# Kernel tuning notes

Hardware: AMD Instinct MI355X
Metric: run time of the kernel (lower is better)

The kernel has to match this reference:

```python
import jax, jax.numpy as jnp
import numpy as np

DIM = 1024
HEADS = 16
HEAD_DIM = DIM // HEADS
HIDDEN = 4 * DIM
EPS = 1e-5


def layernorm(x, g, b):
    mu = jnp.mean(x, axis=-1, keepdims=True)
    var = jnp.var(x, axis=-1, keepdims=True)
    return (x - mu) * jax.lax.rsqrt(var + EPS) * g + b


def setup_inputs() -> dict:
    key = jax.random.key(0)
    ks = jax.random.split(key, 6)
    B, N = 4, 1024
    s = lambda fan_in: 1.0 / np.sqrt(fan_in)
    return {
        "x": jax.random.normal(ks[0], (B, N, DIM), jnp.float32),
        "ln1_g": jnp.ones((DIM,), jnp.float32),
        "ln1_b": jnp.zeros((DIM,), jnp.float32),
        "qkv_w": jax.random.normal(ks[1], (3 * DIM, DIM), jnp.float32) * s(DIM),
        "qkv_b": jnp.zeros((3 * DIM,), jnp.float32),
        "proj_w": jax.random.normal(ks[2], (DIM, DIM), jnp.float32) * s(DIM),
        "proj_b": jnp.zeros((DIM,), jnp.float32),
        "ln2_g": jnp.ones((DIM,), jnp.float32),
        "ln2_b": jnp.zeros((DIM,), jnp.float32),
        "fc1_w": jax.random.normal(ks[3], (HIDDEN, DIM), jnp.float32) * s(DIM),
        "fc1_b": jnp.zeros((HIDDEN,), jnp.float32),
        "fc2_w": jax.random.normal(ks[4], (DIM, HIDDEN), jnp.float32) * s(HIDDEN),
        "fc2_b": jnp.zeros((DIM,), jnp.float32),
    }


def reference(x, ln1_g, ln1_b, qkv_w, qkv_b, proj_w, proj_b,
              ln2_g, ln2_b, fc1_w, fc1_b, fc2_w, fc2_b):
    B, N, C = x.shape
    scale = HEAD_DIM ** -0.5

    # --- attention branch ---
    h = layernorm(x, ln1_g, ln1_b)
    qkv = h @ qkv_w.T + qkv_b                      # [B,N,3C]
    qkv = qkv.reshape(B, N, 3, HEADS, HEAD_DIM)
    q = qkv[:, :, 0].transpose(0, 2, 1, 3) * scale  # [B,H,N,D]
    k = qkv[:, :, 1].transpose(0, 2, 1, 3)
    v = qkv[:, :, 2].transpose(0, 2, 1, 3)
    attn = jax.nn.softmax(jnp.einsum('bhnd,bhmd->bhnm', q, k), axis=-1)
    o = jnp.einsum('bhnm,bhmd->bhnd', attn, v)      # [B,H,N,D]
    o = o.transpose(0, 2, 1, 3).reshape(B, N, C)
    x = x + (o @ proj_w.T + proj_b)

    # --- mlp branch ---
    h = layernorm(x, ln2_g, ln2_b)
    h = jax.nn.gelu(h @ fc1_w.T + fc1_b, approximate=False)
    x = x + (h @ fc2_w.T + fc2_b)
    return x
```

## Files before the change

kernel.cpp:

```cpp
#include <hip/hip_runtime.h>
#include <math.h>

#define DIM 1024
#define HEADS 16
#define HEAD_DIM 64
#define HIDDEN 4096
#define NSEQ 1024
#define BATCH 4
#define TOKENS (BATCH * NSEQ)
#define EPS 1e-5f

typedef __bf16 bf16;
typedef __bf16 bf16x4 __attribute__((ext_vector_type(4)));
typedef __bf16 bf16x8 __attribute__((ext_vector_type(8)));
typedef float f32x4 __attribute__((ext_vector_type(4)));

#define AS1 __attribute__((address_space(1)))
#define AS3 __attribute__((address_space(3)))

__global__ __launch_bounds__(256) void cvt_kernel(const float* __restrict__ s,
                                                  bf16* __restrict__ d) {
    const int i = (blockIdx.x * 256 + threadIdx.x) * 4;
    const float4 v = *(const float4*)(s + i);
    bf16x4 o = {(bf16)v.x, (bf16)v.y, (bf16)v.z, (bf16)v.w};
    *(bf16x4*)(d + i) = o;
}

__global__ __launch_bounds__(256) void ln_kernel(const float* __restrict__ x,
                                                 const float* __restrict__ g,
                                                 const float* __restrict__ b,
                                                 bf16* __restrict__ out) {
    const int t = blockIdx.x;
    const int tid = threadIdx.x;
    const float* row = x + (size_t)t * DIM;
    float v[4];
    float s1 = 0.f, s2 = 0.f;
#pragma unroll
    for (int i = 0; i < 4; i++) {
        v[i] = row[tid + i * 256];
        s1 += v[i];
        s2 += v[i] * v[i];
    }
    __shared__ float w1[4], w2[4];
#pragma unroll
    for (int off = 32; off > 0; off >>= 1) {
        s1 += __shfl_down(s1, off, 64);
        s2 += __shfl_down(s2, off, 64);
    }
    const int wave = tid >> 6;
    if ((tid & 63) == 0) { w1[wave] = s1; w2[wave] = s2; }
    __syncthreads();
    const float sum = w1[0] + w1[1] + w1[2] + w1[3];
    const float ssq = w2[0] + w2[1] + w2[2] + w2[3];
    const float mu = sum * (1.0f / DIM);
    const float var = ssq * (1.0f / DIM) - mu * mu;
    const float rstd = rsqrtf(var + EPS);
    bf16* orow = out + (size_t)t * DIM;
#pragma unroll
    for (int i = 0; i < 4; i++) {
        const int idx = tid + i * 256;
        orow[idx] = (bf16)((v[i] - mu) * rstd * g[idx] + b[idx]);
    }
}

#define ACT_NONE 0
#define ACT_GELU 1

template <int ACT, bool RES, bool OUT_BF16, bool VT>
__global__ __launch_bounds__(256) void mfma_gemm(const bf16* __restrict__ A,
                                                 const bf16* __restrict__ W,
                                                 const float* __restrict__ bias,
                                                 const float* __restrict__ res,
                                                 void* __restrict__ Cout,
                                                 bf16* __restrict__ vTout,
                                                 int M, int N, int K) {
    __shared__ __align__(16) bf16 As[128 * 32];
    __shared__ __align__(16) bf16 Bs[128 * 32];

    const int tid = threadIdx.x;
    const int w = tid >> 6, lane = tid & 63;
    const int bm = blockIdx.y * 128, bn = blockIdx.x * 128;

    const bf16* pa = A + (size_t)(bm + (tid >> 2)) * K + (tid & 3) * 8;
    const bf16* pb = W + (size_t)(bn + (tid >> 2)) * K + (tid & 3) * 8;
    const size_t rowskip = (size_t)64 * K;
    char* ldsA = (char*)As + (w << 10);
    char* ldsB = (char*)Bs + (w << 10);

    const int wm = (w & 1) * 64, wn = (w >> 1) * 64;
    const int fm = lane & 15, fk = (lane >> 4) * 8;
    const bf16* aoff = As + (wm + fm) * 32 + fk;
    const bf16* boff = Bs + (wn + fm) * 32 + fk;

    f32x4 acc[4][4] = {};

    for (int kk = 0; kk < K; kk += 32) {
        __builtin_amdgcn_global_load_lds((const AS1 void*)pa, (AS3 void*)ldsA, 16, 0, 0);
        __builtin_amdgcn_global_load_lds((const AS1 void*)(pa + rowskip), (AS3 void*)(ldsA + 4096), 16, 0, 0);
        __builtin_amdgcn_global_load_lds((const AS1 void*)pb, (AS3 void*)ldsB, 16, 0, 0);
        __builtin_amdgcn_global_load_lds((const AS1 void*)(pb + rowskip), (AS3 void*)(ldsB + 4096), 16, 0, 0);
        pa += 32; pb += 32;
        __syncthreads();

        bf16x8 af[4], bfr[4];
#pragma unroll
        for (int t = 0; t < 4; t++) af[t] = *(const bf16x8*)(aoff + t * 16 * 32);
#pragma unroll
        for (int t = 0; t < 4; t++) bfr[t] = *(const bf16x8*)(boff + t * 16 * 32);
#pragma unroll
        for (int mt = 0; mt < 4; mt++)
#pragma unroll
            for (int nt = 0; nt < 4; nt++)
                acc[mt][nt] = __builtin_amdgcn_mfma_f32_16x16x32_bf16(af[mt], bfr[nt], acc[mt][nt], 0, 0, 0);
        __syncthreads();
    }

    const int cn = bn + wn + fm;
    const int rm = bm + wm + (lane >> 4) * 4;
    float bv[4];
#pragma unroll
    for (int nt = 0; nt < 4; nt++) bv[nt] = bias[cn + nt * 16];

    if (VT && bn >= 2048) {
        const int dg0 = cn - 2048;
#pragma unroll
        for (int mt = 0; mt < 4; mt++) {
            const int mrow = rm + mt * 16;
            const int bI = mrow >> 10, j0 = mrow & 1023;
#pragma unroll
            for (int nt = 0; nt < 4; nt++) {
                const int dg = dg0 + nt * 16;
                bf16x4 v4 = {(bf16)(acc[mt][nt][0] + bv[nt]), (bf16)(acc[mt][nt][1] + bv[nt]),
                             (bf16)(acc[mt][nt][2] + bv[nt]), (bf16)(acc[mt][nt][3] + bv[nt])};
                *(bf16x4*)(vTout + ((size_t)(bI * 1024 + dg)) * 1024 + j0) = v4;
            }
        }
        return;
    }

#pragma unroll
    for (int mt = 0; mt < 4; mt++) {
#pragma unroll
        for (int r = 0; r < 4; r++) {
            const size_t rowoff = (size_t)(rm + mt * 16 + r) * N;
#pragma unroll
            for (int nt = 0; nt < 4; nt++) {
                float val = acc[mt][nt][r] + bv[nt];
                if (ACT == ACT_GELU) val = 0.5f * val * (1.0f + erff(val * 0.70710678118654752f));
                if (RES) val += res[rowoff + cn + nt * 16];
                if (OUT_BF16) ((bf16*)Cout)[rowoff + cn + nt * 16] = (bf16)val;
                else          ((float*)Cout)[rowoff + cn + nt * 16] = val;
            }
        }
    }
}

__global__ __launch_bounds__(256) void fattn_mfma(const bf16* __restrict__ qkv,
                                                  const bf16* __restrict__ vT,
                                                  bf16* __restrict__ out) {
    __shared__ __align__(16) bf16 Ks[64 * 64];
    __shared__ __align__(16) bf16 Vt[64 * 64];
    __shared__ __align__(16) bf16 Ps[64 * 68];

    const int bid = blockIdx.x;
    const int qt = bid & 15;
    const int h = (bid >> 4) & 15;
    const int b = bid >> 8;
    const int tid = threadIdx.x;
    const int w = tid >> 6, lane = tid & 63;
    const int li = lane & 15, g = lane >> 4;

    bf16x8 aQ[2];
    {
        const size_t tok = (size_t)b * NSEQ + qt * 64 + w * 16 + li;
#pragma unroll
        for (int ks = 0; ks < 2; ks++)
            aQ[ks] = *(const bf16x8*)(qkv + tok * (3 * DIM) + h * HEAD_DIM + g * 8 + 32 * ks);
    }

    float mrun[4] = {-INFINITY, -INFINITY, -INFINITY, -INFINITY};
    float lrun[4] = {0.f, 0.f, 0.f, 0.f};
    f32x4 o[4] = {};

    const int idx0 = w * 128 + lane;
    const int idx1 = idx0 + 64;
    const int jl0 = idx0 >> 3, c0 = (idx0 & 7) ^ (jl0 & 7);
    const int jl1 = idx1 >> 3, c1 = (idx1 & 7) ^ (jl1 & 7);
    bf16* ldsK0 = Ks + (size_t)(w * 128) * 8;
    bf16* ldsK1 = Ks + (size_t)(w * 128 + 64) * 8;
    bf16* ldsV0 = Vt + (size_t)(w * 128) * 8;
    bf16* ldsV1 = Vt + (size_t)(w * 128 + 64) * 8;
    const bf16* kbase = qkv + (size_t)b * NSEQ * (3 * DIM) + DIM + h * HEAD_DIM;
    const bf16* vbase = vT + ((size_t)b * DIM + h * HEAD_DIM) * NSEQ;

    for (int k0 = 0; k0 < NSEQ; k0 += 64) {
        __syncthreads();
        __builtin_amdgcn_global_load_lds((const AS1 void*)(kbase + (size_t)(k0 + jl0) * (3 * DIM) + c0 * 8),
                                         (AS3 void*)ldsK0, 16, 0, 0);
        __builtin_amdgcn_global_load_lds((const AS1 void*)(kbase + (size_t)(k0 + jl1) * (3 * DIM) + c1 * 8),
                                         (AS3 void*)ldsK1, 16, 0, 0);
        __builtin_amdgcn_global_load_lds((const AS1 void*)(vbase + (size_t)jl0 * NSEQ + k0 + c0 * 8),
                                         (AS3 void*)ldsV0, 16, 0, 0);
        __builtin_amdgcn_global_load_lds((const AS1 void*)(vbase + (size_t)jl1 * NSEQ + k0 + c1 * 8),
                                         (AS3 void*)ldsV1, 16, 0, 0);
        __syncthreads();

        f32x4 s[4] = {};
#pragma unroll
        for (int ks = 0; ks < 2; ks++) {
#pragma unroll
            for (int nt = 0; nt < 4; nt++) {
                const int j = li + 16 * nt;
                const int p = (g + 4 * ks) ^ (j & 7);
                bf16x8 bK = *(const bf16x8*)(Ks + j * 64 + p * 8);
                s[nt] = __builtin_amdgcn_mfma_f32_16x16x32_bf16(aQ[ks], bK, s[nt], 0, 0, 0);
            }
        }
#pragma unroll
        for (int nt = 0; nt < 4; nt++) s[nt] *= 0.125f;

        float m4[4], rs[4], alpha[4];
#pragma unroll
        for (int r = 0; r < 4; r++)
            m4[r] = fmaxf(fmaxf(s[0][r], s[1][r]), fmaxf(s[2][r], s[3][r]));
#pragma unroll
        for (int mask = 1; mask < 16; mask <<= 1)
#pragma unroll
            for (int r = 0; r < 4; r++) m4[r] = fmaxf(m4[r], __shfl_xor(m4[r], mask, 64));
#pragma unroll
        for (int r = 0; r < 4; r++) {
            const float mn = fmaxf(mrun[r], m4[r]);
            alpha[r] = __expf(mrun[r] - mn);
            mrun[r] = mn;
        }
#pragma unroll
        for (int r = 0; r < 4; r++) rs[r] = 0.f;
#pragma unroll
        for (int nt = 0; nt < 4; nt++) {
#pragma unroll
            for (int r = 0; r < 4; r++) {
                const float p = __expf(s[nt][r] - mrun[r]);
                rs[r] += p;
                Ps[(w * 16 + g * 4 + r) * 68 + li + 16 * nt] = (bf16)p;
            }
        }
#pragma unroll
        for (int mask = 1; mask < 16; mask <<= 1)
#pragma unroll
            for (int r = 0; r < 4; r++) rs[r] += __shfl_xor(rs[r], mask, 64);
#pragma unroll
        for (int r = 0; r < 4; r++) lrun[r] = lrun[r] * alpha[r] + rs[r];
#pragma unroll
        for (int nt = 0; nt < 4; nt++)
#pragma unroll
            for (int r = 0; r < 4; r++) o[nt][r] *= alpha[r];

        bf16x8 aP[2];
#pragma unroll
        for (int ks = 0; ks < 2; ks++) {
            const int off = (w * 16 + li) * 68 + g * 8 + 32 * ks;
            bf16x4 lo = *(const bf16x4*)(Ps + off);
            bf16x4 hi = *(const bf16x4*)(Ps + off + 4);
            aP[ks] = bf16x8{lo[0], lo[1], lo[2], lo[3], hi[0], hi[1], hi[2], hi[3]};
        }
#pragma unroll
        for (int ks = 0; ks < 2; ks++) {
#pragma unroll
            for (int nt = 0; nt < 4; nt++) {
                const int d = li + 16 * nt;
                const int p = (g + 4 * ks) ^ (d & 7);
                bf16x8 bV = *(const bf16x8*)(Vt + d * 64 + p * 8);
                o[nt] = __builtin_amdgcn_mfma_f32_16x16x32_bf16(aP[ks], bV, o[nt], 0, 0, 0);
            }
        }
    }

    float linv[4];
#pragma unroll
    for (int r = 0; r < 4; r++) linv[r] = 1.0f / lrun[r];
    const size_t tok0 = (size_t)b * NSEQ + qt * 64 + w * 16 + g * 4;
#pragma unroll
    for (int r = 0; r < 4; r++) {
#pragma unroll
        for (int nt = 0; nt < 4; nt++)
            out[(tok0 + r) * DIM + h * HEAD_DIM + 16 * nt + li] = (bf16)(o[nt][r] * linv[r]);
    }
}

extern "C" void kernel_launch(void* const* d_in, const int* in_sizes, int n_in,
                              void* d_out, int out_size, void* d_ws, size_t ws_size,
                              hipStream_t stream) {
    const float* x      = (const float*)d_in[0];
    const float* ln1_g  = (const float*)d_in[1];
    const float* ln1_b  = (const float*)d_in[2];
    const float* qkv_w  = (const float*)d_in[3];
    const float* qkv_b  = (const float*)d_in[4];
    const float* proj_w = (const float*)d_in[5];
    const float* proj_b = (const float*)d_in[6];
    const float* ln2_g  = (const float*)d_in[7];
    const float* ln2_b  = (const float*)d_in[8];
    const float* fc1_w  = (const float*)d_in[9];
    const float* fc1_b  = (const float*)d_in[10];
    const float* fc2_w  = (const float*)d_in[11];
    const float* fc2_b  = (const float*)d_in[12];
    float* out = (float*)d_out;

    char* p = (char*)d_ws;
    bf16*  h_bf    = (bf16*)p;  p += (size_t)TOKENS * DIM * 2;
    bf16*  attn_bf = (bf16*)p;  p += (size_t)TOKENS * DIM * 2;
    bf16*  ffn_bf  = (bf16*)p;  p += (size_t)TOKENS * HIDDEN * 2;
    bf16*  qkv_bf  = (bf16*)p;  p += (size_t)TOKENS * 3 * DIM * 2;
    bf16*  vT_bf   = (bf16*)p;  p += (size_t)BATCH * DIM * NSEQ * 2;
    bf16*  wq_bf   = (bf16*)p;  p += (size_t)3 * DIM * DIM * 2;
    bf16*  wp_bf   = (bf16*)p;  p += (size_t)DIM * DIM * 2;
    bf16*  w1_bf   = (bf16*)p;  p += (size_t)HIDDEN * DIM * 2;
    bf16*  w2_bf   = (bf16*)p;  p += (size_t)DIM * HIDDEN * 2;

    cvt_kernel<<<3 * DIM * DIM / 1024, 256, 0, stream>>>(qkv_w, wq_bf);
    cvt_kernel<<<DIM * DIM / 1024, 256, 0, stream>>>(proj_w, wp_bf);
    cvt_kernel<<<HIDDEN * DIM / 1024, 256, 0, stream>>>(fc1_w, w1_bf);
    cvt_kernel<<<DIM * HIDDEN / 1024, 256, 0, stream>>>(fc2_w, w2_bf);

    ln_kernel<<<TOKENS, 256, 0, stream>>>(x, ln1_g, ln1_b, h_bf);
    mfma_gemm<ACT_NONE, false, true, true><<<dim3(3 * DIM / 128, TOKENS / 128), 256, 0, stream>>>(
        h_bf, wq_bf, qkv_b, nullptr, qkv_bf, vT_bf, TOKENS, 3 * DIM, DIM);
    fattn_mfma<<<BATCH * HEADS * (NSEQ / 64), 256, 0, stream>>>(qkv_bf, vT_bf, attn_bf);
    mfma_gemm<ACT_NONE, true, false, false><<<dim3(DIM / 128, TOKENS / 128), 256, 0, stream>>>(
        attn_bf, wp_bf, proj_b, x, out, nullptr, TOKENS, DIM, DIM);
    ln_kernel<<<TOKENS, 256, 0, stream>>>(out, ln2_g, ln2_b, h_bf);
    mfma_gemm<ACT_GELU, false, true, false><<<dim3(HIDDEN / 128, TOKENS / 128), 256, 0, stream>>>(
        h_bf, w1_bf, fc1_b, nullptr, ffn_bf, nullptr, TOKENS, HIDDEN, DIM);
    mfma_gemm<ACT_NONE, true, false, false><<<dim3(DIM / 128, TOKENS / 128), 256, 0, stream>>>(
        ffn_bf, w2_bf, fc2_b, out, out, nullptr, TOKENS, DIM, HIDDEN);
}
```

Baseline: 423.5 us.

## Add split-K with atomic accumulation for narrow GEMMs and fuse weight conversions

Merges the four weight-conversion launches into one kernel that dispatches by index range. Splits the K loop of the proj and fc2 GEMMs in two along grid z, which doubles the block count (256 to 512) on the N=1024 outputs to fill more CUs. Partial results are accumulated into the fp32 output with atomicAdd. The residual is seeded by a device-to-device memcpy of x into out before the proj GEMM. The cost is extra atomic traffic on every output element and the copy itself.

```diff
diff --git a/kernel.cpp b/kernel.cpp
--- a/kernel.cpp
+++ b/kernel.cpp
@@ -18,12 +18,24 @@
 #define AS1 __attribute__((address_space(1)))
 #define AS3 __attribute__((address_space(3)))
 
-__global__ __launch_bounds__(256) void cvt_kernel(const float* __restrict__ s,
-                                                  bf16* __restrict__ d) {
-    const int i = (blockIdx.x * 256 + threadIdx.x) * 4;
-    const float4 v = *(const float4*)(s + i);
+__global__ __launch_bounds__(256) void cvt4_kernel(const float* __restrict__ s0,
+                                                   const float* __restrict__ s1,
+                                                   const float* __restrict__ s2,
+                                                   const float* __restrict__ s3,
+                                                   bf16* __restrict__ d0,
+                                                   bf16* __restrict__ d1,
+                                                   bf16* __restrict__ d2,
+                                                   bf16* __restrict__ d3) {
+    size_t q = (size_t)blockIdx.x * 256 + threadIdx.x;
+    const float* s;
+    bf16* d;
+    if (q < 786432) { s = s0; d = d0; }
+    else if (q < 786432 + 262144) { q -= 786432; s = s1; d = d1; }
+    else if (q < 786432 + 262144 + 1048576) { q -= 786432 + 262144; s = s2; d = d2; }
+    else { q -= 786432 + 262144 + 1048576; s = s3; d = d3; }
+    const float4 v = *(const float4*)(s + q * 4);
     bf16x4 o = {(bf16)v.x, (bf16)v.y, (bf16)v.z, (bf16)v.w};
-    *(bf16x4*)(d + i) = o;
+    *(bf16x4*)(d + q * 4) = o;
 }
 
 __global__ __launch_bounds__(256) void ln_kernel(const float* __restrict__ x,
@@ -66,7 +78,7 @@
 #define ACT_NONE 0
 #define ACT_GELU 1
 
-template <int ACT, bool RES, bool OUT_BF16, bool VT>
+template <int ACT, bool RES, bool OUT_BF16, bool VT, int SPLITK>
 __global__ __launch_bounds__(256) void mfma_gemm(const bf16* __restrict__ A,
                                                  const bf16* __restrict__ W,
                                                  const float* __restrict__ bias,
@@ -80,9 +92,11 @@
     const int tid = threadIdx.x;
     const int w = tid >> 6, lane = tid & 63;
     const int bm = blockIdx.y * 128, bn = blockIdx.x * 128;
-
-    const bf16* pa = A + (size_t)(bm + (tid >> 2)) * K + (tid & 3) * 8;
-    const bf16* pb = W + (size_t)(bn + (tid >> 2)) * K + (tid & 3) * 8;
+    const int kseg = K / SPLITK;
+    const int k0 = (SPLITK > 1) ? blockIdx.z * kseg : 0;
+
+    const bf16* pa = A + (size_t)(bm + (tid >> 2)) * K + k0 + (tid & 3) * 8;
+    const bf16* pb = W + (size_t)(bn + (tid >> 2)) * K + k0 + (tid & 3) * 8;
     const size_t rowskip = (size_t)64 * K;
     char* ldsA = (char*)As + (w << 10);
     char* ldsB = (char*)Bs + (w << 10);
@@ -94,7 +108,7 @@
 
     f32x4 acc[4][4] = {};
 
-    for (int kk = 0; kk < K; kk += 32) {
+    for (int kk = 0; kk < kseg; kk += 32) {
         __builtin_amdgcn_global_load_lds((const AS1 void*)pa, (AS3 void*)ldsA, 16, 0, 0);
         __builtin_amdgcn_global_load_lds((const AS1 void*)(pa + rowskip), (AS3 void*)(ldsA + 4096), 16, 0, 0);
         __builtin_amdgcn_global_load_lds((const AS1 void*)pb, (AS3 void*)ldsB, 16, 0, 0);
@@ -119,7 +133,23 @@
     const int rm = bm + wm + (lane >> 4) * 4;
     float bv[4];
 #pragma unroll
-    for (int nt = 0; nt < 4; nt++) bv[nt] = bias[cn + nt * 16];
+    for (int nt = 0; nt < 4; nt++)
+        bv[nt] = (SPLITK > 1 && blockIdx.z != 0) ? 0.f : bias[cn + nt * 16];
+
+    if (SPLITK > 1) {
+        float* outp = (float*)Cout;
+#pragma unroll
+        for (int mt = 0; mt < 4; mt++) {
+#pragma unroll
+            for (int r = 0; r < 4; r++) {
+                const size_t rowoff = (size_t)(rm + mt * 16 + r) * N;
+#pragma unroll
+                for (int nt = 0; nt < 4; nt++)
+                    atomicAdd(outp + rowoff + cn + nt * 16, acc[mt][nt][r] + bv[nt]);
+            }
+        }
+        return;
+    }
 
     if (VT && bn >= 2048) {
         const int dg0 = cn - 2048;
@@ -316,20 +346,19 @@
     bf16*  w1_bf   = (bf16*)p;  p += (size_t)HIDDEN * DIM * 2;
     bf16*  w2_bf   = (bf16*)p;  p += (size_t)DIM * HIDDEN * 2;
 
-    cvt_kernel<<<3 * DIM * DIM / 1024, 256, 0, stream>>>(qkv_w, wq_bf);
-    cvt_kernel<<<DIM * DIM / 1024, 256, 0, stream>>>(proj_w, wp_bf);
-    cvt_kernel<<<HIDDEN * DIM / 1024, 256, 0, stream>>>(fc1_w, w1_bf);
-    cvt_kernel<<<DIM * HIDDEN / 1024, 256, 0, stream>>>(fc2_w, w2_bf);
+    cvt4_kernel<<<(3145728 + 1048576 + 4194304 + 4194304) / 1024, 256, 0, stream>>>(
+        qkv_w, proj_w, fc1_w, fc2_w, wq_bf, wp_bf, w1_bf, w2_bf);
 
     ln_kernel<<<TOKENS, 256, 0, stream>>>(x, ln1_g, ln1_b, h_bf);
-    mfma_gemm<ACT_NONE, false, true, true><<<dim3(3 * DIM / 128, TOKENS / 128), 256, 0, stream>>>(
+    mfma_gemm<ACT_NONE, false, true, true, 1><<<dim3(3 * DIM / 128, TOKENS / 128), 256, 0, stream>>>(
         h_bf, wq_bf, qkv_b, nullptr, qkv_bf, vT_bf, TOKENS, 3 * DIM, DIM);
     fattn_mfma<<<BATCH * HEADS * (NSEQ / 64), 256, 0, stream>>>(qkv_bf, vT_bf, attn_bf);
-    mfma_gemm<ACT_NONE, true, false, false><<<dim3(DIM / 128, TOKENS / 128), 256, 0, stream>>>(
-        attn_bf, wp_bf, proj_b, x, out, nullptr, TOKENS, DIM, DIM);
+    hipMemcpyAsync(out, x, (size_t)TOKENS * DIM * sizeof(float), hipMemcpyDeviceToDevice, stream);
+    mfma_gemm<ACT_NONE, false, false, false, 2><<<dim3(DIM / 128, TOKENS / 128, 2), 256, 0, stream>>>(
+        attn_bf, wp_bf, proj_b, nullptr, out, nullptr, TOKENS, DIM, DIM);
     ln_kernel<<<TOKENS, 256, 0, stream>>>(out, ln2_g, ln2_b, h_bf);
-    mfma_gemm<ACT_GELU, false, true, false><<<dim3(HIDDEN / 128, TOKENS / 128), 256, 0, stream>>>(
+    mfma_gemm<ACT_GELU, false, true, false, 1><<<dim3(HIDDEN / 128, TOKENS / 128), 256, 0, stream>>>(
         h_bf, w1_bf, fc1_b, nullptr, ffn_bf, nullptr, TOKENS, HIDDEN, DIM);
-    mfma_gemm<ACT_NONE, true, false, false><<<dim3(DIM / 128, TOKENS / 128), 256, 0, stream>>>(
-        ffn_bf, w2_bf, fc2_b, out, out, nullptr, TOKENS, DIM, HIDDEN);
-}
+    mfma_gemm<ACT_NONE, false, false, false, 2><<<dim3(DIM / 128, TOKENS / 128, 2), 256, 0, stream>>>(
+        ffn_bf, w2_bf, fc2_b, nullptr, out, nullptr, TOKENS, DIM, HIDDEN);
+}
```

After: 414.7 us. -2.1%, faster.
